# Kernel tuning notes

Measured on AMD Instinct MI355X. Metric: run time of the kernel, lower is better.

## Reference

```python
import jax, jax.numpy as jnp
import numpy as np

N = 50000      # num nodes
E = 800000     # num edges
D = 64         # in_dim = hid_dim = out_dim
K = 8          # propagation hops (num_layers)
ALPHA = 0.6


def setup_inputs() -> dict:
    key = jax.random.key(0)
    ks = jax.random.split(key, 6)
    s = 1.0 / np.sqrt(D)
    return {
        "x": jax.random.normal(ks[0], (N, D), jnp.float32),
        "w_conv": jax.random.normal(ks[1], (D, D), jnp.float32) * s,
        "b_conv": jnp.zeros((D,), jnp.float32),
        "w1": jax.random.normal(ks[2], (D, D), jnp.float32) * s,
        "b1": jnp.zeros((D,), jnp.float32),
        "w2": jax.random.normal(ks[3], (D, D), jnp.float32) * s,
        "b2": jnp.zeros((D,), jnp.float32),
        "edge_index": jax.random.randint(ks[4], (2, E), 0, N, jnp.int64),
    }


def _gcn_norm(edge_index, num_nodes):
    # add self loops, symmetric normalization D^-1/2 (A+I) D^-1/2
    loop = jnp.arange(num_nodes, dtype=edge_index.dtype)
    src = jnp.concatenate([edge_index[0], loop])
    dst = jnp.concatenate([edge_index[1], loop])
    ones = jnp.ones(src.shape[0], jnp.float32)
    deg = jax.ops.segment_sum(ones, dst, num_segments=num_nodes)
    dinv = jnp.where(deg > 0, jax.lax.rsqrt(deg), 0.0)
    norm = dinv[src] * dinv[dst]  # [E+N]
    return src, dst, norm


def reference(x, w_conv, b_conv, w1, b1, w2, b2, edge_index):
    num_nodes = x.shape[0]
    src, dst, norm = _gcn_norm(edge_index, num_nodes)
    # SSGConv: h = alpha*x + (1-alpha)/K * sum_k A_hat^k x
    h = ALPHA * x
    xk = x
    coef = (1.0 - ALPHA) / K
    for _ in range(K):
        xk = jax.ops.segment_sum(norm[:, None] * xk[src], dst, num_segments=num_nodes)
        h = h + coef * xk
    h = h @ w_conv.T + b_conv        # SSGConv's internal Linear
    h = jax.nn.relu(h)               # F.relu(conv1(...))
    h = jax.nn.relu(h @ w1.T + b1)   # lin1 + relu (dropout p=0, eval)
    return h @ w2.T + b2             # lin2
```

## Files before the change

### kernel.cpp

```cpp
#include <hip/hip_runtime.h>

#define DD 64
#define ALPHA 0.6f
#define KHOPS 8
#define WP 72

typedef __attribute__((ext_vector_type(8))) short bf16x8;
typedef __attribute__((ext_vector_type(4))) float f32x4;

static __device__ __forceinline__ unsigned short f2bf(float f) {
    unsigned int u = __float_as_uint(f);
    unsigned int r = (u + 0x7FFFu + ((u >> 16) & 1u)) >> 16;
    return (unsigned short)r;
}
static __device__ __forceinline__ float bf2f(unsigned short h) {
    return __uint_as_float(((unsigned int)h) << 16);
}
static __device__ __forceinline__ unsigned int pack2bf(float lo, float hi) {
    return (unsigned int)f2bf(lo) | ((unsigned int)f2bf(hi) << 16);
}

__global__ __launch_bounds__(256) void deg_count_kernel(const int* __restrict__ dst,
                                                        int* __restrict__ cnt, int e) {
    int i = blockIdx.x * blockDim.x + threadIdx.x;
    if (i < e) atomicAdd(&cnt[dst[i]], 1);
}

__global__ __launch_bounds__(256) void dinv_kernel(const int* __restrict__ cnt,
                                                   float* __restrict__ dinv, int n) {
    int i = blockIdx.x * blockDim.x + threadIdx.x;
    if (i < n) dinv[i] = rsqrtf((float)(cnt[i] + 1));
}

__global__ __launch_bounds__(256) void scan1_kernel(const int* __restrict__ cnt,
                                                    int* __restrict__ partials, int n) {
    int i = blockIdx.x * 256 + threadIdx.x;
    int v = (i < n) ? cnt[i] : 0;
    #pragma unroll
    for (int off = 1; off < 64; off <<= 1) v += __shfl_down(v, off, 64);
    __shared__ int ws[4];
    if ((threadIdx.x & 63) == 0) ws[threadIdx.x >> 6] = v;
    __syncthreads();
    if (threadIdx.x == 0) partials[blockIdx.x] = ws[0] + ws[1] + ws[2] + ws[3];
}

__global__ __launch_bounds__(1024) void scan2_kernel(int* __restrict__ partials, int nb) {
    __shared__ int s[1024];
    int t = threadIdx.x;
    int v = (t < nb) ? partials[t] : 0;
    s[t] = v;
    __syncthreads();
    for (int off = 1; off < 1024; off <<= 1) {
        int tmp = (t >= off) ? s[t - off] : 0;
        __syncthreads();
        s[t] += tmp;
        __syncthreads();
    }
    if (t < nb) partials[t] = s[t] - v;
}

__global__ __launch_bounds__(256) void scan3_kernel(const int* __restrict__ cnt,
                                                    const int* __restrict__ partials,
                                                    int* __restrict__ rowptr,
                                                    int* __restrict__ cursor, int n) {
    int t = threadIdx.x;
    int i = blockIdx.x * 256 + t;
    int v = (i < n) ? cnt[i] : 0;
    int lane = t & 63;
    int incl = v;
    #pragma unroll
    for (int off = 1; off < 64; off <<= 1) {
        int u = __shfl_up(incl, off, 64);
        if (lane >= off) incl += u;
    }
    __shared__ int wsum[4];
    if (lane == 63) wsum[t >> 6] = incl;
    __syncthreads();
    int woff = 0;
    for (int w = 0; w < (t >> 6); ++w) woff += wsum[w];
    int excl = incl - v + woff + partials[blockIdx.x];
    if (i < n) { rowptr[i] = excl; cursor[i] = excl; }
    if (i == n - 1) rowptr[n] = excl + v;
}

__global__ __launch_bounds__(256) void fill_kernel(const int* __restrict__ src,
                                                   const int* __restrict__ dst,
                                                   const float* __restrict__ dinv,
                                                   int* __restrict__ cursor,
                                                   int2* __restrict__ ecsr, int e) {
    int i = blockIdx.x * blockDim.x + threadIdx.x;
    if (i >= e) return;
    int s = src[i], d = dst[i];
    int pos = atomicAdd(&cursor[d], 1);
    float w = dinv[s] * dinv[d];
    ecsr[pos] = make_int2(s, __float_as_int(w));
}

__global__ __launch_bounds__(256) void init_kernel(const float4* __restrict__ x,
                                                   float4* __restrict__ h,
                                                   ushort4* __restrict__ xb, int n4) {
    int i = blockIdx.x * blockDim.x + threadIdx.x;
    if (i >= n4) return;
    float4 v = x[i];
    h[i] = make_float4(ALPHA * v.x, ALPHA * v.y, ALPHA * v.z, ALPHA * v.w);
    ushort4 b;
    b.x = f2bf(v.x); b.y = f2bf(v.y); b.z = f2bf(v.z); b.w = f2bf(v.w);
    xb[i] = b;
}

static __device__ __forceinline__ void fma8(float* acc, uint4 v, float w) {
    acc[0] += w * __uint_as_float(v.x << 16);
    acc[1] += w * __uint_as_float(v.x & 0xffff0000u);
    acc[2] += w * __uint_as_float(v.y << 16);
    acc[3] += w * __uint_as_float(v.y & 0xffff0000u);
    acc[4] += w * __uint_as_float(v.z << 16);
    acc[5] += w * __uint_as_float(v.z & 0xffff0000u);
    acc[6] += w * __uint_as_float(v.w << 16);
    acc[7] += w * __uint_as_float(v.w & 0xffff0000u);
}

template <int DO_H>
__global__ __launch_bounds__(256) void hop_kernel(const int* __restrict__ rowptr,
                                                  const int2* __restrict__ ecsr,
                                                  const float* __restrict__ dinv,
                                                  const unsigned short* __restrict__ xin,
                                                  unsigned short* __restrict__ xout,
                                                  float* __restrict__ h,
                                                  float coef, int n) {
    int wid = (blockIdx.x * blockDim.x + threadIdx.x) >> 6;
    if (wid >= n) return;
    int lane = threadIdx.x & 63;
    int g = lane >> 3;
    int s = lane & 7;
    int node = wid;

    int e0 = rowptr[node];
    int e1 = rowptr[node + 1];

    float acc[8] = {0.f, 0.f, 0.f, 0.f, 0.f, 0.f, 0.f, 0.f};
    float xprev[8];

    if (g == 0) {
        float di = dinv[node];
        float w = di * di;
        uint4 v = *(const uint4*)(xin + (size_t)node * 64 + s * 8);
        xprev[0] = __uint_as_float(v.x << 16);
        xprev[1] = __uint_as_float(v.x & 0xffff0000u);
        xprev[2] = __uint_as_float(v.y << 16);
        xprev[3] = __uint_as_float(v.y & 0xffff0000u);
        xprev[4] = __uint_as_float(v.z << 16);
        xprev[5] = __uint_as_float(v.z & 0xffff0000u);
        xprev[6] = __uint_as_float(v.w << 16);
        xprev[7] = __uint_as_float(v.w & 0xffff0000u);
        #pragma unroll
        for (int j = 0; j < 8; ++j) acc[j] = w * xprev[j];
    }

    int deg = e1 - e0;
    int niter = (deg + 7) >> 3;
    int i = 0;
    for (; i + 1 < niter; i += 2) {
        int eA = e0 + (i << 3) + g;
        int eB = eA + 8;
        int2 edA = ecsr[eA];
        bool vB = eB < e1;
        int2 edB = ecsr[vB ? eB : (e1 - 1)];
        uint4 va = *(const uint4*)(xin + (size_t)edA.x * 64 + s * 8);
        uint4 vb = *(const uint4*)(xin + (size_t)edB.x * 64 + s * 8);
        fma8(acc, va, __int_as_float(edA.y));
        fma8(acc, vb, vB ? __int_as_float(edB.y) : 0.0f);
    }
    if (i < niter) {
        int eA = e0 + (i << 3) + g;
        bool vA = eA < e1;
        int2 edA = ecsr[vA ? eA : (e1 - 1)];
        uint4 va = *(const uint4*)(xin + (size_t)edA.x * 64 + s * 8);
        fma8(acc, va, vA ? __int_as_float(edA.y) : 0.0f);
    }

    #pragma unroll
    for (int off = 8; off < 64; off <<= 1) {
        #pragma unroll
        for (int j = 0; j < 8; ++j) acc[j] += __shfl_xor(acc[j], off, 64);
    }

    if (g == 0) {
        uint4 o;
        o.x = pack2bf(acc[0], acc[1]);
        o.y = pack2bf(acc[2], acc[3]);
        o.z = pack2bf(acc[4], acc[5]);
        o.w = pack2bf(acc[6], acc[7]);
        *(uint4*)(xout + (size_t)node * 64 + s * 8) = o;
        if (DO_H) {
            float* hp = h + (size_t)node * 64 + s * 8;
            float4 h0 = *(float4*)hp;
            float4 h1 = *(float4*)(hp + 4);
            h0.x += coef * (xprev[0] + acc[0]);
            h0.y += coef * (xprev[1] + acc[1]);
            h0.z += coef * (xprev[2] + acc[2]);
            h0.w += coef * (xprev[3] + acc[3]);
            h1.x += coef * (xprev[4] + acc[4]);
            h1.y += coef * (xprev[5] + acc[5]);
            h1.z += coef * (xprev[6] + acc[6]);
            h1.w += coef * (xprev[7] + acc[7]);
            *(float4*)hp = h0;
            *(float4*)(hp + 4) = h1;
        }
    }
}

__global__ __launch_bounds__(256) void mlp_mfma_kernel(const float* __restrict__ hin,
                                                       const float* __restrict__ wc,
                                                       const float* __restrict__ bc,
                                                       const float* __restrict__ w1,
                                                       const float* __restrict__ b1,
                                                       const float* __restrict__ w2,
                                                       const float* __restrict__ b2,
                                                       float* __restrict__ out, int n) {
    __shared__ unsigned short wlds[3][64][WP];
    __shared__ unsigned short xlds[64][WP];
    int t = threadIdx.x;

    const float* wm[3] = {wc, w1, w2};
    #pragma unroll
    for (int m = 0; m < 3; ++m) {
        const float4* w4 = (const float4*)wm[m];
        #pragma unroll
        for (int k = 0; k < 4; ++k) {
            int fid = t + k * 256;
            int j = fid >> 4, c4 = fid & 15;
            float4 v = w4[fid];
            *(uint2*)&wlds[m][j][c4 * 4] =
                make_uint2(pack2bf(v.x, v.y), pack2bf(v.z, v.w));
        }
    }

    int r0 = blockIdx.x * 64;
    const float4* h4 = (const float4*)hin;
    #pragma unroll
    for (int k = 0; k < 4; ++k) {
        int fid = t + k * 256;
        int r = fid >> 4, c4 = fid & 15;
        int gr = r0 + r;
        float4 v = (gr < n) ? h4[(size_t)gr * 16 + c4]
                            : make_float4(0.f, 0.f, 0.f, 0.f);
        *(uint2*)&xlds[r][c4 * 4] = make_uint2(pack2bf(v.x, v.y), pack2bf(v.z, v.w));
    }
    __syncthreads();

    int lane = t & 63;
    int wv = t >> 6;
    int rbase = wv * 16;
    int lr = lane & 15;
    int kg = lane >> 4;
    const float* bias[3] = {bc, b1, b2};

    #pragma unroll
    for (int m = 0; m < 3; ++m) {
        bf16x8 a0 = *(bf16x8*)&xlds[rbase + lr][kg * 8];
        bf16x8 a1 = *(bf16x8*)&xlds[rbase + lr][32 + kg * 8];
        #pragma unroll
        for (int ct = 0; ct < 4; ++ct) {
            bf16x8 bv0 = *(bf16x8*)&wlds[m][ct * 16 + lr][kg * 8];
            bf16x8 bv1 = *(bf16x8*)&wlds[m][ct * 16 + lr][32 + kg * 8];
            f32x4 acc = {0.f, 0.f, 0.f, 0.f};
            acc = __builtin_amdgcn_mfma_f32_16x16x32_bf16(a0, bv0, acc, 0, 0, 0);
            acc = __builtin_amdgcn_mfma_f32_16x16x32_bf16(a1, bv1, acc, 0, 0, 0);
            float bb = bias[m][ct * 16 + lr];
            if (m < 2) {
                #pragma unroll
                for (int rg = 0; rg < 4; ++rg) {
                    float v = fmaxf(acc[rg] + bb, 0.0f);
                    xlds[rbase + kg * 4 + rg][ct * 16 + lr] = f2bf(v);
                }
            } else {
                #pragma unroll
                for (int rg = 0; rg < 4; ++rg) {
                    int gr = r0 + rbase + kg * 4 + rg;
                    if (gr < n) out[(size_t)gr * 64 + ct * 16 + lr] = acc[rg] + bb;
                }
            }
        }
    }
}

extern "C" void kernel_launch(void* const* d_in, const int* in_sizes, int n_in,
                              void* d_out, int out_size, void* d_ws, size_t ws_size,
                              hipStream_t stream) {
    const float* x      = (const float*)d_in[0];
    const float* w_conv = (const float*)d_in[1];
    const float* b_conv = (const float*)d_in[2];
    const float* w1     = (const float*)d_in[3];
    const float* b1     = (const float*)d_in[4];
    const float* w2     = (const float*)d_in[5];
    const float* b2     = (const float*)d_in[6];
    const int*   ei     = (const int*)d_in[7];

    int n = in_sizes[0] / DD;
    int e = in_sizes[7] / 2;
    const int* src = ei;
    const int* dst = ei + e;

    char* wsb = (char*)d_ws;
    const size_t SLOT = 256 * 1024;
    int*   cnt      = (int*)(wsb + 0 * SLOT);
    float* dinv     = (float*)(wsb + 1 * SLOT);
    int*   rowptr   = (int*)(wsb + 2 * SLOT);
    int*   cursor   = (int*)(wsb + 3 * SLOT);
    int*   partials = (int*)(wsb + 4 * SLOT);
    int2*  ecsr     = (int2*)(wsb + 5 * SLOT);
    unsigned short* xb0 = (unsigned short*)(wsb + 5 * SLOT + (size_t)e * 8);
    unsigned short* xb1 = xb0 + (size_t)n * DD;
    float* h = (float*)d_out;

    const int B = 256;
    int n4 = n * (DD / 4);
    int nb = (n + 255) / 256;

    hipMemsetAsync(cnt, 0, (size_t)n * sizeof(int), stream);
    deg_count_kernel<<<(e + B - 1) / B, B, 0, stream>>>(dst, cnt, e);
    dinv_kernel<<<(n + B - 1) / B, B, 0, stream>>>(cnt, dinv, n);
    scan1_kernel<<<nb, B, 0, stream>>>(cnt, partials, n);
    scan2_kernel<<<1, 1024, 0, stream>>>(partials, nb);
    scan3_kernel<<<nb, B, 0, stream>>>(cnt, partials, rowptr, cursor, n);
    fill_kernel<<<(e + B - 1) / B, B, 0, stream>>>(src, dst, dinv, cursor, ecsr, e);

    init_kernel<<<(n4 + B - 1) / B, B, 0, stream>>>(
        (const float4*)x, (float4*)h, (ushort4*)xb0, n4);

    float coef = (1.0f - ALPHA) / (float)KHOPS;
    int hblocks = (int)(((size_t)n * 64 + B - 1) / B);

    unsigned short* cur = xb0;
    unsigned short* nxt = xb1;
    for (int k = 1; k <= KHOPS; ++k) {
        if (k % 2 == 0)
            hop_kernel<1><<<hblocks, B, 0, stream>>>(rowptr, ecsr, dinv, cur, nxt, h,
                                                     coef, n);
        else
            hop_kernel<0><<<hblocks, B, 0, stream>>>(rowptr, ecsr, dinv, cur, nxt, h,
                                                     coef, n);
        unsigned short* tmp = cur; cur = nxt; nxt = tmp;
    }

    mlp_mfma_kernel<<<(n + 63) / 64, B, 0, stream>>>(h, w_conv, b_conv, w1, b1,
                                                     w2, b2, (float*)d_out, n);
}
```

Baseline: 292.6 us.

## Propagate degree-prescaled features to drop per-edge weights from CSR

Rewrites the normalized propagation as y = D^-1/2 x, so each hop sums neighbor rows unweighted and scales by dinv^2 once per node. The CSR then stores only source indices (4 bytes per edge instead of 8), which cuts edge-list traffic and removes per-edge multiplies in the gather loop. The h accumulation is recovered with per-node sqrt(deg) and dinv factors. Rounding now happens on the rescaled values in bf16, which changes numerics slightly, and the fill kernel uses nontemporal stores.

```diff
diff --git a/kernel.cpp b/kernel.cpp
--- a/kernel.cpp
+++ b/kernel.cpp
@@ -13,9 +13,6 @@
     unsigned int r = (u + 0x7FFFu + ((u >> 16) & 1u)) >> 16;
     return (unsigned short)r;
 }
-static __device__ __forceinline__ float bf2f(unsigned short h) {
-    return __uint_as_float(((unsigned int)h) << 16);
-}
 static __device__ __forceinline__ unsigned int pack2bf(float lo, float hi) {
     return (unsigned int)f2bf(lo) | ((unsigned int)f2bf(hi) << 16);
 }
@@ -27,9 +24,12 @@
 }
 
 __global__ __launch_bounds__(256) void dinv_kernel(const int* __restrict__ cnt,
-                                                   float* __restrict__ dinv, int n) {
+                                                   float2* __restrict__ dinvr, int n) {
     int i = blockIdx.x * blockDim.x + threadIdx.x;
-    if (i < n) dinv[i] = rsqrtf((float)(cnt[i] + 1));
+    if (i < n) {
+        float d = (float)(cnt[i] + 1);
+        dinvr[i] = make_float2(rsqrtf(d), sqrtf(d));
+    }
 }
 
 __global__ __launch_bounds__(256) void scan1_kernel(const int* __restrict__ cnt,
@@ -85,46 +85,48 @@
 
 __global__ __launch_bounds__(256) void fill_kernel(const int* __restrict__ src,
                                                    const int* __restrict__ dst,
-                                                   const float* __restrict__ dinv,
                                                    int* __restrict__ cursor,
-                                                   int2* __restrict__ ecsr, int e) {
+                                                   int* __restrict__ esrc, int e) {
     int i = blockIdx.x * blockDim.x + threadIdx.x;
     if (i >= e) return;
     int s = src[i], d = dst[i];
     int pos = atomicAdd(&cursor[d], 1);
-    float w = dinv[s] * dinv[d];
-    ecsr[pos] = make_int2(s, __float_as_int(w));
+    __builtin_nontemporal_store(s, &esrc[pos]);
 }
 
 __global__ __launch_bounds__(256) void init_kernel(const float4* __restrict__ x,
+                                                   const float2* __restrict__ dinvr,
                                                    float4* __restrict__ h,
-                                                   ushort4* __restrict__ xb, int n4) {
+                                                   ushort4* __restrict__ yb, int n4) {
     int i = blockIdx.x * blockDim.x + threadIdx.x;
     if (i >= n4) return;
+    int row = i >> 4;
+    float di = dinvr[row].x;
     float4 v = x[i];
     h[i] = make_float4(ALPHA * v.x, ALPHA * v.y, ALPHA * v.z, ALPHA * v.w);
     ushort4 b;
-    b.x = f2bf(v.x); b.y = f2bf(v.y); b.z = f2bf(v.z); b.w = f2bf(v.w);
-    xb[i] = b;
-}
-
-static __device__ __forceinline__ void fma8(float* acc, uint4 v, float w) {
-    acc[0] += w * __uint_as_float(v.x << 16);
-    acc[1] += w * __uint_as_float(v.x & 0xffff0000u);
-    acc[2] += w * __uint_as_float(v.y << 16);
-    acc[3] += w * __uint_as_float(v.y & 0xffff0000u);
-    acc[4] += w * __uint_as_float(v.z << 16);
-    acc[5] += w * __uint_as_float(v.z & 0xffff0000u);
-    acc[6] += w * __uint_as_float(v.w << 16);
-    acc[7] += w * __uint_as_float(v.w & 0xffff0000u);
+    b.x = f2bf(di * v.x); b.y = f2bf(di * v.y);
+    b.z = f2bf(di * v.z); b.w = f2bf(di * v.w);
+    yb[i] = b;
+}
+
+static __device__ __forceinline__ void add8(float* acc, uint4 v) {
+    acc[0] += __uint_as_float(v.x << 16);
+    acc[1] += __uint_as_float(v.x & 0xffff0000u);
+    acc[2] += __uint_as_float(v.y << 16);
+    acc[3] += __uint_as_float(v.y & 0xffff0000u);
+    acc[4] += __uint_as_float(v.z << 16);
+    acc[5] += __uint_as_float(v.z & 0xffff0000u);
+    acc[6] += __uint_as_float(v.w << 16);
+    acc[7] += __uint_as_float(v.w & 0xffff0000u);
 }
 
 template <int DO_H>
 __global__ __launch_bounds__(256) void hop_kernel(const int* __restrict__ rowptr,
-                                                  const int2* __restrict__ ecsr,
-                                                  const float* __restrict__ dinv,
-                                                  const unsigned short* __restrict__ xin,
-                                                  unsigned short* __restrict__ xout,
+                                                  const int* __restrict__ esrc,
+                                                  const float2* __restrict__ dinvr,
+                                                  const unsigned short* __restrict__ yin,
+                                                  unsigned short* __restrict__ yout,
                                                   float* __restrict__ h,
                                                   float coef, int n) {
     int wid = (blockIdx.x * blockDim.x + threadIdx.x) >> 6;
@@ -138,22 +140,22 @@
     int e1 = rowptr[node + 1];
 
     float acc[8] = {0.f, 0.f, 0.f, 0.f, 0.f, 0.f, 0.f, 0.f};
-    float xprev[8];
+    float yprev[8];
+    float2 dr;
 
     if (g == 0) {
-        float di = dinv[node];
-        float w = di * di;
-        uint4 v = *(const uint4*)(xin + (size_t)node * 64 + s * 8);
-        xprev[0] = __uint_as_float(v.x << 16);
-        xprev[1] = __uint_as_float(v.x & 0xffff0000u);
-        xprev[2] = __uint_as_float(v.y << 16);
-        xprev[3] = __uint_as_float(v.y & 0xffff0000u);
-        xprev[4] = __uint_as_float(v.z << 16);
-        xprev[5] = __uint_as_float(v.z & 0xffff0000u);
-        xprev[6] = __uint_as_float(v.w << 16);
-        xprev[7] = __uint_as_float(v.w & 0xffff0000u);
+        dr = dinvr[node];
+        uint4 v = *(const uint4*)(yin + (size_t)node * 64 + s * 8);
+        yprev[0] = __uint_as_float(v.x << 16);
+        yprev[1] = __uint_as_float(v.x & 0xffff0000u);
+        yprev[2] = __uint_as_float(v.y << 16);
+        yprev[3] = __uint_as_float(v.y & 0xffff0000u);
+        yprev[4] = __uint_as_float(v.z << 16);
+        yprev[5] = __uint_as_float(v.z & 0xffff0000u);
+        yprev[6] = __uint_as_float(v.w << 16);
+        yprev[7] = __uint_as_float(v.w & 0xffff0000u);
         #pragma unroll
-        for (int j = 0; j < 8; ++j) acc[j] = w * xprev[j];
+        for (int j = 0; j < 8; ++j) acc[j] = yprev[j];
     }
 
     int deg = e1 - e0;
@@ -162,20 +164,22 @@
     for (; i + 1 < niter; i += 2) {
         int eA = e0 + (i << 3) + g;
         int eB = eA + 8;
-        int2 edA = ecsr[eA];
+        int sA = esrc[eA];
         bool vB = eB < e1;
-        int2 edB = ecsr[vB ? eB : (e1 - 1)];
-        uint4 va = *(const uint4*)(xin + (size_t)edA.x * 64 + s * 8);
-        uint4 vb = *(const uint4*)(xin + (size_t)edB.x * 64 + s * 8);
-        fma8(acc, va, __int_as_float(edA.y));
-        fma8(acc, vb, vB ? __int_as_float(edB.y) : 0.0f);
+        int sB = esrc[vB ? eB : (e1 - 1)];
+        uint4 va = *(const uint4*)(yin + (size_t)sA * 64 + s * 8);
+        uint4 vb = *(const uint4*)(yin + (size_t)sB * 64 + s * 8);
+        if (!vB) vb = make_uint4(0u, 0u, 0u, 0u);
+        add8(acc, va);
+        add8(acc, vb);
     }
     if (i < niter) {
         int eA = e0 + (i << 3) + g;
         bool vA = eA < e1;
-        int2 edA = ecsr[vA ? eA : (e1 - 1)];
-        uint4 va = *(const uint4*)(xin + (size_t)edA.x * 64 + s * 8);
-        fma8(acc, va, vA ? __int_as_float(edA.y) : 0.0f);
+        int sA = esrc[vA ? eA : (e1 - 1)];
+        uint4 va = *(const uint4*)(yin + (size_t)sA * 64 + s * 8);
+        if (!vA) va = make_uint4(0u, 0u, 0u, 0u);
+        add8(acc, va);
     }
 
     #pragma unroll
@@ -185,24 +189,27 @@
     }
 
     if (g == 0) {
+        float di = dr.x;
+        float d2 = di * di;
         uint4 o;
-        o.x = pack2bf(acc[0], acc[1]);
-        o.y = pack2bf(acc[2], acc[3]);
-        o.z = pack2bf(acc[4], acc[5]);
-        o.w = pack2bf(acc[6], acc[7]);
-        *(uint4*)(xout + (size_t)node * 64 + s * 8) = o;
+        o.x = pack2bf(d2 * acc[0], d2 * acc[1]);
+        o.y = pack2bf(d2 * acc[2], d2 * acc[3]);
+        o.z = pack2bf(d2 * acc[4], d2 * acc[5]);
+        o.w = pack2bf(d2 * acc[6], d2 * acc[7]);
+        *(uint4*)(yout + (size_t)node * 64 + s * 8) = o;
         if (DO_H) {
+            float rd = dr.y;
             float* hp = h + (size_t)node * 64 + s * 8;
             float4 h0 = *(float4*)hp;
             float4 h1 = *(float4*)(hp + 4);
-            h0.x += coef * (xprev[0] + acc[0]);
-            h0.y += coef * (xprev[1] + acc[1]);
-            h0.z += coef * (xprev[2] + acc[2]);
-            h0.w += coef * (xprev[3] + acc[3]);
-            h1.x += coef * (xprev[4] + acc[4]);
-            h1.y += coef * (xprev[5] + acc[5]);
-            h1.z += coef * (xprev[6] + acc[6]);
-            h1.w += coef * (xprev[7] + acc[7]);
+            h0.x += coef * (rd * yprev[0] + di * acc[0]);
+            h0.y += coef * (rd * yprev[1] + di * acc[1]);
+            h0.z += coef * (rd * yprev[2] + di * acc[2]);
+            h0.w += coef * (rd * yprev[3] + di * acc[3]);
+            h1.x += coef * (rd * yprev[4] + di * acc[4]);
+            h1.y += coef * (rd * yprev[5] + di * acc[5]);
+            h1.z += coef * (rd * yprev[6] + di * acc[6]);
+            h1.w += coef * (rd * yprev[7] + di * acc[7]);
             *(float4*)hp = h0;
             *(float4*)(hp + 4) = h1;
         }
@@ -302,15 +309,14 @@
     const int* dst = ei + e;
 
     char* wsb = (char*)d_ws;
-    const size_t SLOT = 256 * 1024;
-    int*   cnt      = (int*)(wsb + 0 * SLOT);
-    float* dinv     = (float*)(wsb + 1 * SLOT);
-    int*   rowptr   = (int*)(wsb + 2 * SLOT);
-    int*   cursor   = (int*)(wsb + 3 * SLOT);
-    int*   partials = (int*)(wsb + 4 * SLOT);
-    int2*  ecsr     = (int2*)(wsb + 5 * SLOT);
-    unsigned short* xb0 = (unsigned short*)(wsb + 5 * SLOT + (size_t)e * 8);
-    unsigned short* xb1 = xb0 + (size_t)n * DD;
+    int*    cnt      = (int*)(wsb + 0);
+    float2* dinvr    = (float2*)(wsb + 256 * 1024);
+    int*    rowptr   = (int*)(wsb + 768 * 1024);
+    int*    cursor   = (int*)(wsb + 1024 * 1024);
+    int*    partials = (int*)(wsb + 1280 * 1024);
+    int*    esrc     = (int*)(wsb + 1344 * 1024);
+    unsigned short* yb0 = (unsigned short*)(wsb + 1344 * 1024 + (size_t)e * 4);
+    unsigned short* yb1 = yb0 + (size_t)n * DD;
     float* h = (float*)d_out;
 
     const int B = 256;
@@ -319,26 +325,26 @@
 
     hipMemsetAsync(cnt, 0, (size_t)n * sizeof(int), stream);
     deg_count_kernel<<<(e + B - 1) / B, B, 0, stream>>>(dst, cnt, e);
-    dinv_kernel<<<(n + B - 1) / B, B, 0, stream>>>(cnt, dinv, n);
+    dinv_kernel<<<(n + B - 1) / B, B, 0, stream>>>(cnt, dinvr, n);
     scan1_kernel<<<nb, B, 0, stream>>>(cnt, partials, n);
     scan2_kernel<<<1, 1024, 0, stream>>>(partials, nb);
     scan3_kernel<<<nb, B, 0, stream>>>(cnt, partials, rowptr, cursor, n);
-    fill_kernel<<<(e + B - 1) / B, B, 0, stream>>>(src, dst, dinv, cursor, ecsr, e);
+    fill_kernel<<<(e + B - 1) / B, B, 0, stream>>>(src, dst, cursor, esrc, e);
 
     init_kernel<<<(n4 + B - 1) / B, B, 0, stream>>>(
-        (const float4*)x, (float4*)h, (ushort4*)xb0, n4);
+        (const float4*)x, dinvr, (float4*)h, (ushort4*)yb0, n4);
 
     float coef = (1.0f - ALPHA) / (float)KHOPS;
     int hblocks = (int)(((size_t)n * 64 + B - 1) / B);
 
-    unsigned short* cur = xb0;
-    unsigned short* nxt = xb1;
+    unsigned short* cur = yb0;
+    unsigned short* nxt = yb1;
     for (int k = 1; k <= KHOPS; ++k) {
         if (k % 2 == 0)
-            hop_kernel<1><<<hblocks, B, 0, stream>>>(rowptr, ecsr, dinv, cur, nxt, h,
+            hop_kernel<1><<<hblocks, B, 0, stream>>>(rowptr, esrc, dinvr, cur, nxt, h,
                                                      coef, n);
         else
-            hop_kernel<0><<<hblocks, B, 0, stream>>>(rowptr, ecsr, dinv, cur, nxt, h,
+            hop_kernel<0><<<hblocks, B, 0, stream>>>(rowptr, esrc, dinvr, cur, nxt, h,
                                                      coef, n);
         unsigned short* tmp = cur; cur = nxt; nxt = tmp;
     }
```

Result: slower. 305.6 us (+4.4%).
